# Kernel optimization log

Measured on AMD Instinct MI355X. Metric: run time of the kernel, lower is better.

The kernel has to match this reference:

```python
import jax, jax.numpy as jnp
import numpy as np

N = 128          # num_of_nodes
E = 4096         # directed edges (undirected doubled)
D = N + 2        # node feature dim after node_dim += num_of_nodes
H = 64           # hidden_dim


def _lin_params(key, fan_in, fan_out):
    s = 1.0 / np.sqrt(fan_in)
    kw, kb = jax.random.split(key)
    W = jax.random.uniform(kw, (fan_in, fan_out), jnp.float32, -s, s)
    b = jax.random.uniform(kb, (fan_out,), jnp.float32, -s, s)
    return W, b


def setup_inputs() -> dict:
    key = jax.random.key(0)
    ks = jax.random.split(key, 16)
    x = jax.random.normal(ks[0], (N, D), jnp.float32)
    edge_index = jax.random.randint(ks[1], (2, E), 0, N)
    edge_attr = jax.random.uniform(ks[2], (E, 1), jnp.float32)
    adjacency = jax.random.randint(ks[3], (N, N), 0, 2).astype(jnp.int32)
    # values in {-1, 0, 1}; -1 means node created no packet
    new_packets = jax.random.randint(ks[4], (N,), -1, 2).astype(jnp.float32)
    # conv1 edge MLP: Linear(1, D*H) -> ReLU -> Linear(D*H, D*H)
    W1a, b1a = _lin_params(ks[5], 1, D * H)
    W1b, b1b = _lin_params(ks[6], D * H, D * H)
    Wr1, _ = _lin_params(ks[7], D, H)        # NNConv root weight (no bias)
    bc1 = jnp.zeros((H,), jnp.float32)       # NNConv bias
    # conv2 edge MLP: Linear(1, H) -> ReLU -> Linear(H, H*H)
    W2a, b2a = _lin_params(ks[8], 1, H)
    W2b, b2b = _lin_params(ks[9], H, H * H)
    Wr2, _ = _lin_params(ks[10], H, H)
    bc2 = jnp.zeros((H,), jnp.float32)
    Wout, bout = _lin_params(ks[11], H, N)
    return dict(x=x, edge_index=edge_index, edge_attr=edge_attr,
                adjacency=adjacency, new_packets=new_packets,
                W1a=W1a, b1a=b1a, W1b=W1b, b1b=b1b, Wr1=Wr1, bc1=bc1,
                W2a=W2a, b2a=b2a, W2b=W2b, b2b=b2b, Wr2=Wr2, bc2=bc2,
                Wout=Wout, bout=bout)


def _nnconv(x, src, dst, edge_attr, Wa, ba, Wb, bb, Wr, bias, din, dout):
    # per-edge weight matrices from edge MLP: [E, din, dout]
    theta = (jax.nn.relu(edge_attr @ Wa + ba) @ Wb + bb).reshape(-1, din, dout)
    msg = jnp.einsum('ei,eio->eo', x[src], theta)          # gather + edge matmul
    agg = jax.ops.segment_sum(msg, dst, num_segments=N)     # scatter
    cnt = jax.ops.segment_sum(jnp.ones((msg.shape[0],), msg.dtype), dst,
                              num_segments=N)
    agg = agg / jnp.maximum(cnt, 1.0)[:, None]              # mean aggregation
    return agg + x @ Wr + bias                              # root weight + bias


def reference(x, edge_index, edge_attr, adjacency, new_packets,
              W1a, b1a, W1b, b1b, Wr1, bc1,
              W2a, b2a, W2b, b2b, Wr2, bc2,
              Wout, bout):
    src, dst = edge_index[0], edge_index[1]
    h = jax.nn.relu(_nnconv(x, src, dst, edge_attr, W1a, b1a, W1b, b1b, Wr1, bc1, D, H))
    h = jax.nn.relu(_nnconv(h, src, dst, edge_attr, W2a, b2a, W2b, b2b, Wr2, bc2, H, H))
    logits = h @ Wout + bout                                 # [N, N]
    masked = jnp.where(adjacency != 0, logits, -jnp.inf)
    probs = jax.nn.softmax(masked, axis=1)
    mask = new_packets != -1.0                               # nodes that created packets
    rp = jnp.where(mask[:, None], probs, 0.0)                # zero rows w/o packet
    idx = jnp.arange(N)
    rp = rp.at[idx, idx].add(jnp.where(mask, 0.0, 1.0))      # diag=1 for those rows
    return rp
```

## Files before the change

kernel.cpp:

```cpp
#include <hip/hip_runtime.h>

#define NN 128
#define NE 4096
#define DD 130
#define HH 64
#define KK1 8320
#define CC 256

#define OFF_AGG1 0
#define OFF_AGG2 8192
#define ZERO_F   16384
#define OFF_CNT  16384
#define OFF_XR1  16512
#define OFF_H1   24704
#define OFF_HB2  32896
#define OFF_HR2  41088
#define OFF_H2   49280
#define OFF_G2   57472
#define OFF_SP   581760
#define OFF_SQ   2711680
#define OFF_DP   4841600
#define OFF_DQ   6971520
#define OFF_INT  9101440

__device__ __forceinline__ int event_bin(float a, float c) {
  if (a > 0.f) {
    if (c <= 0.f) { float tt = -c / a; if (tt < 1.f) return (int)(tt * 256.0f); }
  } else if (a < 0.f) {
    if (c > 0.f) { float tt = -c / a; if (tt < 1.f) return (int)ceilf(tt * 256.0f) - 1; }
  }
  return -1;
}

__global__ __launch_bounds__(256) void k_count(const int* __restrict__ ei,
                                               const float* __restrict__ eattr,
                                               const float* __restrict__ W1a,
                                               const float* __restrict__ b1a,
                                               int* __restrict__ e_off,
                                               int* __restrict__ k_off,
                                               int* __restrict__ e_idx,
                                               int* __restrict__ k_idx,
                                               int* __restrict__ base_idx,
                                               int* __restrict__ nbase,
                                               float* __restrict__ cnt) {
  __shared__ int ec[CC], kc[CC], cd[NN];
  __shared__ int eo[CC + 1], ko[CC + 1];
  __shared__ int bcnt;
  int t = threadIdx.x;
  ec[t] = 0; kc[t] = 0;
  if (t < NN) cd[t] = 0;
  if (t == 0) bcnt = 0;
  __syncthreads();
  for (int e = t; e < NE; e += 256) {
    atomicAdd(&cd[ei[NE + e]], 1);
    int c = (int)(eattr[e] * 256.0f); c = c < 0 ? 0 : (c > CC - 1 ? CC - 1 : c);
    atomicAdd(&ec[c], 1);
  }
  for (int k = t; k < KK1; k += 256) {
    int b = event_bin(W1a[k], b1a[k]);
    if (b >= 0) atomicAdd(&kc[b], 1);
    if (b1a[k] > 0.f) { int p = atomicAdd(&bcnt, 1); base_idx[p] = k; }
  }
  __syncthreads();
  if (t == 0) {
    *nbase = bcnt;
    int r = 0;
    for (int c = 0; c < CC; c++) { eo[c] = r; r += ec[c]; } eo[CC] = r;
    r = 0;
    for (int c = 0; c < CC; c++) { ko[c] = r; r += kc[c]; } ko[CC] = r;
  }
  __syncthreads();
  if (t < NN) cnt[t] = (float)cd[t];
  e_off[t] = eo[t]; k_off[t] = ko[t];
  if (t == 0) { e_off[CC] = eo[CC]; k_off[CC] = ko[CC]; }
  ec[t] = eo[t]; kc[t] = ko[t];
  __syncthreads();
  for (int e = t; e < NE; e += 256) {
    int c = (int)(eattr[e] * 256.0f); c = c < 0 ? 0 : (c > CC - 1 ? CC - 1 : c);
    int p = atomicAdd(&ec[c], 1);
    e_idx[p] = e;
  }
  for (int k = t; k < KK1; k += 256) {
    int b = event_bin(W1a[k], b1a[k]);
    if (b >= 0) { int p = atomicAdd(&kc[b], 1); k_idx[p] = k; }
  }
}

__global__ __launch_bounds__(256) void k_small1x(const float* __restrict__ x,
                                                 const float* __restrict__ Wr1,
                                                 float* __restrict__ xr1) {
  int f = blockIdx.x * 256 + threadIdx.x;
  int n = f >> 6, o = f & 63;
  float a = 0.f;
  for (int i = 0; i < DD; i++) a = fmaf(x[n * DD + i], Wr1[i * HH + o], a);
  xr1[f] = a;
}

#define MCOL 33
__global__ __launch_bounds__(256) void k_base(const float* __restrict__ W1a,
                                              const float* __restrict__ b1a,
                                              const float* __restrict__ W1b,
                                              const int* __restrict__ base_idx,
                                              const int* __restrict__ nbase,
                                              float* __restrict__ SP0,
                                              float* __restrict__ SQ0) {
  int t = threadIdx.x;
  int nb = *nbase;
  float rp[MCOL], rq[MCOL];
#pragma unroll
  for (int m = 0; m < MCOL; m++) { rp[m] = 0.f; rq[m] = 0.f; }
  for (int r = blockIdx.x; r < nb; r += gridDim.x) {
    int k = base_idx[r];
    float a = W1a[k], c2 = b1a[k];
    const float* row = &W1b[(long)k * KK1];
#pragma unroll
    for (int m = 0; m < MCOL; m++) {
      int col = t + 256 * m;
      if (col < KK1) {
        float w = row[col];
        rp[m] = fmaf(a, w, rp[m]);
        rq[m] = fmaf(c2, w, rq[m]);
      }
    }
  }
#pragma unroll
  for (int m = 0; m < MCOL; m++) {
    int col = t + 256 * m;
    if (col < KK1) {
      atomicAdd(&SP0[col], rp[m]);
      atomicAdd(&SQ0[col], rq[m]);
    }
  }
}

__global__ __launch_bounds__(256) void k_diff(const float* __restrict__ W1a,
                                              const float* __restrict__ b1a,
                                              const float* __restrict__ W1b,
                                              const int* __restrict__ k_off,
                                              const int* __restrict__ k_idx,
                                              float* __restrict__ DP,
                                              float* __restrict__ DQ) {
  int c = blockIdx.x, t = threadIdx.x;
  int kb = k_off[c], ke = k_off[c + 1];
  float rp[MCOL], rq[MCOL];
#pragma unroll
  for (int m = 0; m < MCOL; m++) { rp[m] = 0.f; rq[m] = 0.f; }
  for (int r = kb; r < ke; ++r) {
    int k = k_idx[r];
    float a = W1a[k], c2 = b1a[k];
    float sa = (a > 0.f) ? a : -a;
    float sc = (a > 0.f) ? c2 : -c2;
    const float* row = &W1b[(long)k * KK1];
#pragma unroll
    for (int m = 0; m < MCOL; m++) {
      int col = t + 256 * m;
      if (col < KK1) {
        float w = row[col];
        rp[m] = fmaf(sa, w, rp[m]);
        rq[m] = fmaf(sc, w, rq[m]);
      }
    }
  }
#pragma unroll
  for (int m = 0; m < MCOL; m++) {
    int col = t + 256 * m;
    if (col < KK1) {
      DP[(long)c * KK1 + col] = rp[m];
      DQ[(long)c * KK1 + col] = rq[m];
    }
  }
}

__global__ __launch_bounds__(256) void k_prefix(float* __restrict__ SP,
                                                float* __restrict__ SQ,
                                                const float* __restrict__ DP,
                                                const float* __restrict__ DQ) {
  int f = blockIdx.x * 256 + threadIdx.x;
  float* S; const float* Dm; int col;
  if (f < KK1) { S = SP; Dm = DP; col = f; }
  else         { S = SQ; Dm = DQ; col = f - KK1; }
  float s = S[col];
  for (int c = 1; c < CC; c++) {
    s += Dm[(long)(c - 1) * KK1 + col];
    S[(long)c * KK1 + col] = s;
  }
}

#define EC 192
#define KC 128
__global__ __launch_bounds__(256) void k_sweep(const float* __restrict__ SP,
                                               const float* __restrict__ SQ,
                                               const float* __restrict__ b1b,
                                               const float* __restrict__ W1a,
                                               const float* __restrict__ b1a,
                                               const float* __restrict__ W1b,
                                               const float* __restrict__ x,
                                               const float* __restrict__ eattr,
                                               const int* __restrict__ ei,
                                               const int* __restrict__ e_off,
                                               const int* __restrict__ e_idx,
                                               const int* __restrict__ k_off,
                                               const int* __restrict__ k_idx,
                                               float* __restrict__ agg1) {
  __shared__ float Pl[KK1], Ql[KK1];
  __shared__ float eas[EC], eas_r[EC];
  __shared__ int eix[EC], eix_r[EC];
  __shared__ float tks[KC], tks_r[KC];
  __shared__ int kix[KC], kix_r[KC];
  int c = blockIdx.x, t = threadIdx.x;
  int eb = e_off[c], ne = e_off[c + 1] - eb; if (ne > EC) ne = EC;
  int kb = k_off[c], nk = k_off[c + 1] - kb; if (nk > KC) nk = KC;
  for (int j = t; j < KK1; j += 256) {
    Pl[j] = SP[(long)c * KK1 + j];
    Ql[j] = SQ[(long)c * KK1 + j] + b1b[j];
  }
  if (t < ne) { int e = e_idx[eb + t]; eix_r[t] = e; eas_r[t] = eattr[e]; }
  if (t < nk) {
    int k = k_idx[kb + t];
    kix_r[t] = k;
    tks_r[t] = -b1a[k] / W1a[k];
  }
  __syncthreads();
  if (t < ne) {
    float key = eas_r[t]; int rk = 0;
    for (int j = 0; j < ne; j++) { float kj = eas_r[j]; rk += (kj < key) || (kj == key && j < t); }
    eas[rk] = key; eix[rk] = eix_r[t];
  }
  if (t < nk) {
    float key = tks_r[t]; int rk = 0;
    for (int j = 0; j < nk; j++) { float kj = tks_r[j]; rk += (kj < key) || (kj == key && j < t); }
    tks[rk] = key; kix[rk] = kix_r[t];
  }
  __syncthreads();
  if (ne == 0) return;
  int ie = 0, ik = 0;
  int q = t >> 6, o = t & 63;
  while (ie < ne) {
    if (ik < nk && tks[ik] < eas[ie]) {
      int k = kix[ik];
      float a = W1a[k], c2 = b1a[k];
      float sa = (a > 0.f) ? a : -a;
      float sc = (a > 0.f) ? c2 : -c2;
      __syncthreads();
      for (int j = t; j < KK1; j += 256) {
        float w = W1b[(long)k * KK1 + j];
        Pl[j] = fmaf(sa, w, Pl[j]);
        Ql[j] = fmaf(sc, w, Ql[j]);
      }
      __syncthreads();
      ik++;
    } else {
      int m = 1;
      while (ie + m < ne && (ik >= nk || eas[ie + m] <= tks[ik])) m++;
      for (int g = 0; g < m; g += 4) {
        int sl = g + q;
        if (sl < m) {
          int e = eix[ie + sl];
          float eav = eas[ie + sl];
          int s = ei[e], d = ei[NE + e];
          const float* xp = &x[s * DD];
          float A = 0.f, B = 0.f;
#pragma unroll 2
          for (int i = 0; i < DD; i++) {
            float xv = xp[i];
            A = fmaf(xv, Pl[i * 64 + o], A);
            B = fmaf(xv, Ql[i * 64 + o], B);
          }
          atomicAdd(&agg1[d * 64 + o], fmaf(eav, A, B));
        }
      }
      ie += m;
    }
  }
}

__global__ __launch_bounds__(256) void k_h(const float* __restrict__ agg,
                                           const float* __restrict__ cnt,
                                           const float* __restrict__ xr,
                                           const float* __restrict__ bc,
                                           float* __restrict__ h) {
  int f = blockIdx.x * 256 + threadIdx.x;
  int n = f >> 6, o = f & 63;
  float c = fmaxf(cnt[n], 1.f);
  h[f] = fmaxf(0.f, agg[f] / c + xr[f] + bc[o]);
}

__global__ __launch_bounds__(256) void k_g2(const float* __restrict__ h1,
                                            const float* __restrict__ W2b,
                                            float* __restrict__ G2) {
  int f = blockIdx.x * 256 + threadIdx.x;
  int s = f >> 12, k = (f >> 6) & 63, o = f & 63;
  const float* hp = &h1[s * 64];
  const float* wp = &W2b[k * 4096 + o];
  float a = 0.f;
  for (int i = 0; i < 64; i++) a = fmaf(hp[i], wp[i * 64], a);
  G2[f] = a;
}

__global__ __launch_bounds__(256) void k_small2(const float* __restrict__ h1,
                                                const float* __restrict__ b2b,
                                                const float* __restrict__ Wr2,
                                                float* __restrict__ hb2,
                                                float* __restrict__ hr2) {
  int f = blockIdx.x * 256 + threadIdx.x;
  int n = f >> 6, o = f & 63;
  float a = 0.f, b = 0.f;
  for (int i = 0; i < 64; i++) {
    float hv = h1[n * 64 + i];
    a = fmaf(hv, b2b[i * 64 + o], a);
    b = fmaf(hv, Wr2[i * 64 + o], b);
  }
  hb2[f] = a; hr2[f] = b;
}

__global__ __launch_bounds__(256) void k_consume2(const float* __restrict__ G2,
                                                  const float* __restrict__ W2a,
                                                  const float* __restrict__ b2a,
                                                  const float* __restrict__ eattr,
                                                  const int* __restrict__ ei,
                                                  const float* __restrict__ hb2,
                                                  float* __restrict__ agg2) {
  __shared__ float wa[64], wb[64];
  int t = threadIdx.x;
  if (t < 64) { wa[t] = W2a[t]; wb[t] = b2a[t]; }
  __syncthreads();
  int f = blockIdx.x * 256 + t;
  int e = f >> 6, o = f & 63;
  int s = ei[e], d = ei[NE + e];
  float ev = eattr[e];
  float a = hb2[s * 64 + o];
  const float* gp = &G2[s * 4096 + o];
  for (int k = 0; k < 64; k++) {
    float u = fmaxf(0.f, fmaf(ev, wa[k], wb[k]));
    a = fmaf(u, gp[k * 64], a);
  }
  atomicAdd(&agg2[d * 64 + o], a);
}

__global__ __launch_bounds__(128) void k_out(const float* __restrict__ h2,
                                             const float* __restrict__ Wout,
                                             const float* __restrict__ bout,
                                             const int* __restrict__ adj,
                                             const float* __restrict__ npk,
                                             float* __restrict__ out) {
  __shared__ float hs[64];
  __shared__ float redm[2], reds[2];
  int n = blockIdx.x, j = threadIdx.x;
  if (j < 64) hs[j] = h2[n * 64 + j];
  __syncthreads();
  float l = bout[j];
  for (int k = 0; k < 64; k++) l = fmaf(hs[k], Wout[k * 128 + j], l);
  bool am = adj[n * 128 + j] != 0;
  float lm = am ? l : -3.0e38f;
  float m = lm;
  for (int off = 32; off >= 1; off >>= 1) m = fmaxf(m, __shfl_xor(m, off, 64));
  int wid = j >> 6;
  if ((j & 63) == 0) redm[wid] = m;
  __syncthreads();
  m = fmaxf(redm[0], redm[1]);
  float p = am ? expf(lm - m) : 0.f;
  float sv = p;
  for (int off = 32; off >= 1; off >>= 1) sv += __shfl_xor(sv, off, 64);
  if ((j & 63) == 0) reds[wid] = sv;
  __syncthreads();
  sv = reds[0] + reds[1];
  float prob = p / sv;
  bool haspkt = (npk[n] != -1.0f);
  out[n * 128 + j] = haspkt ? prob : ((j == n) ? 1.f : 0.f);
}

extern "C" void kernel_launch(void* const* d_in, const int* in_sizes, int n_in,
                              void* d_out, int out_size, void* d_ws, size_t ws_size,
                              hipStream_t stream) {
  const float* x    = (const float*)d_in[0];
  const int*   ei   = (const int*)  d_in[1];
  const float* ea   = (const float*)d_in[2];
  const int*   adj  = (const int*)  d_in[3];
  const float* npk  = (const float*)d_in[4];
  const float* W1a  = (const float*)d_in[5];
  const float* b1a  = (const float*)d_in[6];
  const float* W1b  = (const float*)d_in[7];
  const float* b1b  = (const float*)d_in[8];
  const float* Wr1  = (const float*)d_in[9];
  const float* bc1  = (const float*)d_in[10];
  const float* W2a  = (const float*)d_in[11];
  const float* b2a  = (const float*)d_in[12];
  const float* W2b  = (const float*)d_in[13];
  const float* b2b  = (const float*)d_in[14];
  const float* Wr2  = (const float*)d_in[15];
  const float* bc2  = (const float*)d_in[16];
  const float* Wout = (const float*)d_in[17];
  const float* bout = (const float*)d_in[18];

  float* ws = (float*)d_ws;
  int*   ip = (int*)(ws + OFF_INT);
  int* e_off    = ip;
  int* k_off    = ip + 257;
  int* e_idx    = ip + 514;
  int* k_idx    = ip + 4610;
  int* base_idx = ip + 12930;
  int* nbase    = ip + 21250;

  hipMemsetAsync(ws, 0, ZERO_F * sizeof(float), stream);
  hipMemsetAsync(ws + OFF_SP, 0, KK1 * sizeof(float), stream);
  hipMemsetAsync(ws + OFF_SQ, 0, KK1 * sizeof(float), stream);

  k_count<<<1, 256, 0, stream>>>(ei, ea, W1a, b1a, e_off, k_off, e_idx, k_idx,
                                 base_idx, nbase, ws + OFF_CNT);
  k_small1x<<<32, 256, 0, stream>>>(x, Wr1, ws + OFF_XR1);
  k_base<<<256, 256, 0, stream>>>(W1a, b1a, W1b, base_idx, nbase,
                                  ws + OFF_SP, ws + OFF_SQ);
  k_diff<<<CC, 256, 0, stream>>>(W1a, b1a, W1b, k_off, k_idx, ws + OFF_DP, ws + OFF_DQ);
  k_prefix<<<65, 256, 0, stream>>>(ws + OFF_SP, ws + OFF_SQ, ws + OFF_DP, ws + OFF_DQ);
  k_sweep<<<CC, 256, 0, stream>>>(ws + OFF_SP, ws + OFF_SQ, b1b, W1a, b1a, W1b,
                                  x, ea, ei, e_off, e_idx, k_off, k_idx, ws + OFF_AGG1);
  k_h<<<32, 256, 0, stream>>>(ws + OFF_AGG1, ws + OFF_CNT, ws + OFF_XR1, bc1, ws + OFF_H1);
  k_g2<<<2048, 256, 0, stream>>>(ws + OFF_H1, W2b, ws + OFF_G2);
  k_small2<<<32, 256, 0, stream>>>(ws + OFF_H1, b2b, Wr2, ws + OFF_HB2, ws + OFF_HR2);
  k_consume2<<<1024, 256, 0, stream>>>(ws + OFF_G2, W2a, b2a, ea, ei, ws + OFF_HB2,
                                       ws + OFF_AGG2);
  k_h<<<32, 256, 0, stream>>>(ws + OFF_AGG2, ws + OFF_CNT, ws + OFF_HR2, bc2, ws + OFF_H2);
  k_out<<<128, 128, 0, stream>>>(ws + OFF_H2, Wout, bout, adj, npk, (float*)d_out);
}
```

Before: 650.1 us.

## Parallelize prefix scan, split sweep by output half, CSR-gather conv2 aggregation

Replaces the serial 256-step column prefix over DP/DQ with a two-pass segmented scan (segment totals, then per-segment scan), so the grid grows by a factor of NSEG. k_sweep is split across two output halves, which halves its LDS footprint and doubles the block count, and b1b is now folded into SQ0 by a new init kernel. k_count also builds a destination-sorted edge permutation, and k_consume2 uses it to reduce per node in LDS, replacing global atomics with plain stores. The cost is extra launches, redundant reads of segment totals, and duplicated sorting and x loads per sweep half.

```diff
diff --git a/kernel.cpp b/kernel.cpp
--- a/kernel.cpp
+++ b/kernel.cpp
@@ -6,22 +6,26 @@
 #define HH 64
 #define KK1 8320
 #define CC 256
+#define NSEG 16
+#define SEGC 16
 
 #define OFF_AGG1 0
-#define OFF_AGG2 8192
-#define ZERO_F   16384
-#define OFF_CNT  16384
-#define OFF_XR1  16512
-#define OFF_H1   24704
-#define OFF_HB2  32896
-#define OFF_HR2  41088
-#define OFF_H2   49280
+#define ZERO_F   8192
+#define OFF_CNT  8192
+#define OFF_XR1  8320
+#define OFF_H1   16512
+#define OFF_HB2  24704
+#define OFF_HR2  32896
+#define OFF_H2   41088
+#define OFF_AGG2 49280
 #define OFF_G2   57472
 #define OFF_SP   581760
 #define OFF_SQ   2711680
 #define OFF_DP   4841600
 #define OFF_DQ   6971520
 #define OFF_INT  9101440
+#define OFF_TP   9127040
+#define OFF_TQ   9260160
 
 __device__ __forceinline__ int event_bin(float a, float c) {
   if (a > 0.f) {
@@ -42,9 +46,11 @@
                                                int* __restrict__ k_idx,
                                                int* __restrict__ base_idx,
                                                int* __restrict__ nbase,
+                                               int* __restrict__ d_off,
+                                               int* __restrict__ perm_dst,
                                                float* __restrict__ cnt) {
   __shared__ int ec[CC], kc[CC], cd[NN];
-  __shared__ int eo[CC + 1], ko[CC + 1];
+  __shared__ int eo[CC + 1], ko[CC + 1], doff[NN + 1];
   __shared__ int bcnt;
   int t = threadIdx.x;
   ec[t] = 0; kc[t] = 0;
@@ -68,17 +74,24 @@
     for (int c = 0; c < CC; c++) { eo[c] = r; r += ec[c]; } eo[CC] = r;
     r = 0;
     for (int c = 0; c < CC; c++) { ko[c] = r; r += kc[c]; } ko[CC] = r;
-  }
-  __syncthreads();
-  if (t < NN) cnt[t] = (float)cd[t];
+    r = 0;
+    for (int n = 0; n < NN; n++) { doff[n] = r; r += cd[n]; } doff[NN] = r;
+  }
+  __syncthreads();
+  if (t < NN) { cnt[t] = (float)cd[t]; d_off[t] = doff[t]; }
+  if (t == 0) d_off[NN] = doff[NN];
   e_off[t] = eo[t]; k_off[t] = ko[t];
   if (t == 0) { e_off[CC] = eo[CC]; k_off[CC] = ko[CC]; }
   ec[t] = eo[t]; kc[t] = ko[t];
+  if (t < NN) cd[t] = doff[t];
   __syncthreads();
   for (int e = t; e < NE; e += 256) {
     int c = (int)(eattr[e] * 256.0f); c = c < 0 ? 0 : (c > CC - 1 ? CC - 1 : c);
     int p = atomicAdd(&ec[c], 1);
     e_idx[p] = e;
+    int d = ei[NE + e];
+    int pd = atomicAdd(&cd[d], 1);
+    perm_dst[pd] = e;
   }
   for (int k = t; k < KK1; k += 256) {
     int b = event_bin(W1a[k], b1a[k]);
@@ -94,6 +107,13 @@
   float a = 0.f;
   for (int i = 0; i < DD; i++) a = fmaf(x[n * DD + i], Wr1[i * HH + o], a);
   xr1[f] = a;
+}
+
+__global__ __launch_bounds__(256) void k_init(const float* __restrict__ b1b,
+                                              float* __restrict__ SP0,
+                                              float* __restrict__ SQ0) {
+  int f = blockIdx.x * 256 + threadIdx.x;
+  if (f < KK1) { SP0[f] = 0.f; SQ0[f] = b1b[f]; }
 }
 
 #define MCOL 33
@@ -171,26 +191,45 @@
   }
 }
 
-__global__ __launch_bounds__(256) void k_prefix(float* __restrict__ SP,
-                                                float* __restrict__ SQ,
-                                                const float* __restrict__ DP,
-                                                const float* __restrict__ DQ) {
-  int f = blockIdx.x * 256 + threadIdx.x;
-  float* S; const float* Dm; int col;
-  if (f < KK1) { S = SP; Dm = DP; col = f; }
-  else         { S = SQ; Dm = DQ; col = f - KK1; }
-  float s = S[col];
-  for (int c = 1; c < CC; c++) {
-    s += Dm[(long)(c - 1) * KK1 + col];
-    S[(long)c * KK1 + col] = s;
+__global__ __launch_bounds__(256) void k_seg(const float* __restrict__ DP,
+                                             const float* __restrict__ DQ,
+                                             float* __restrict__ TP,
+                                             float* __restrict__ TQ) {
+  int f = blockIdx.x * 256 + threadIdx.x;
+  int s = blockIdx.y;
+  const float* Dm; float* T; int col;
+  if (f < KK1) { Dm = DP; T = TP; col = f; }
+  else         { Dm = DQ; T = TQ; col = f - KK1; }
+  float a = 0.f;
+  for (int p = 0; p < SEGC; p++) a += Dm[(long)(s * SEGC + p) * KK1 + col];
+  T[(long)s * KK1 + col] = a;
+}
+
+__global__ __launch_bounds__(256) void k_scan(float* __restrict__ SP,
+                                              float* __restrict__ SQ,
+                                              const float* __restrict__ DP,
+                                              const float* __restrict__ DQ,
+                                              const float* __restrict__ TP,
+                                              const float* __restrict__ TQ) {
+  int f = blockIdx.x * 256 + threadIdx.x;
+  int s = blockIdx.y;
+  float* S; const float* Dm; const float* T; int col;
+  if (f < KK1) { S = SP; Dm = DP; T = TP; col = f; }
+  else         { S = SQ; Dm = DQ; T = TQ; col = f - KK1; }
+  float acc = S[col];
+  for (int sp = 0; sp < s; sp++) acc += T[(long)sp * KK1 + col];
+  for (int p = 0; p < SEGC; p++) {
+    int c = s * SEGC + p;
+    if (c > 0) S[(long)c * KK1 + col] = acc;
+    acc += Dm[(long)c * KK1 + col];
   }
 }
 
 #define EC 192
 #define KC 128
+#define KHW 4160
 __global__ __launch_bounds__(256) void k_sweep(const float* __restrict__ SP,
                                                const float* __restrict__ SQ,
-                                               const float* __restrict__ b1b,
                                                const float* __restrict__ W1a,
                                                const float* __restrict__ b1a,
                                                const float* __restrict__ W1b,
@@ -202,17 +241,20 @@
                                                const int* __restrict__ k_off,
                                                const int* __restrict__ k_idx,
                                                float* __restrict__ agg1) {
-  __shared__ float Pl[KK1], Ql[KK1];
+  __shared__ float Pl[KHW], Ql[KHW];
   __shared__ float eas[EC], eas_r[EC];
   __shared__ int eix[EC], eix_r[EC];
   __shared__ float tks[KC], tks_r[KC];
   __shared__ int kix[KC], kix_r[KC];
-  int c = blockIdx.x, t = threadIdx.x;
+  int c = blockIdx.x, oh = blockIdx.y, t = threadIdx.x;
+  int ob = oh * 32;
   int eb = e_off[c], ne = e_off[c + 1] - eb; if (ne > EC) ne = EC;
   int kb = k_off[c], nk = k_off[c + 1] - kb; if (nk > KC) nk = KC;
-  for (int j = t; j < KK1; j += 256) {
-    Pl[j] = SP[(long)c * KK1 + j];
-    Ql[j] = SQ[(long)c * KK1 + j] + b1b[j];
+  for (int j = t; j < KHW; j += 256) {
+    int i = j >> 5, ol = j & 31;
+    long col = (long)c * KK1 + i * 64 + ob + ol;
+    Pl[j] = SP[col];
+    Ql[j] = SQ[col];
   }
   if (t < ne) { int e = e_idx[eb + t]; eix_r[t] = e; eas_r[t] = eattr[e]; }
   if (t < nk) {
@@ -234,16 +276,18 @@
   __syncthreads();
   if (ne == 0) return;
   int ie = 0, ik = 0;
-  int q = t >> 6, o = t & 63;
+  int q = t >> 5, ol = t & 31;
   while (ie < ne) {
     if (ik < nk && tks[ik] < eas[ie]) {
       int k = kix[ik];
       float a = W1a[k], c2 = b1a[k];
       float sa = (a > 0.f) ? a : -a;
       float sc = (a > 0.f) ? c2 : -c2;
+      const float* row = &W1b[(long)k * KK1 + ob];
       __syncthreads();
-      for (int j = t; j < KK1; j += 256) {
-        float w = W1b[(long)k * KK1 + j];
+      for (int j = t; j < KHW; j += 256) {
+        int i = j >> 5, o2 = j & 31;
+        float w = row[i * 64 + o2];
         Pl[j] = fmaf(sa, w, Pl[j]);
         Ql[j] = fmaf(sc, w, Ql[j]);
       }
@@ -252,7 +296,7 @@
     } else {
       int m = 1;
       while (ie + m < ne && (ik >= nk || eas[ie + m] <= tks[ik])) m++;
-      for (int g = 0; g < m; g += 4) {
+      for (int g = 0; g < m; g += 8) {
         int sl = g + q;
         if (sl < m) {
           int e = eix[ie + sl];
@@ -263,10 +307,10 @@
 #pragma unroll 2
           for (int i = 0; i < DD; i++) {
             float xv = xp[i];
-            A = fmaf(xv, Pl[i * 64 + o], A);
-            B = fmaf(xv, Ql[i * 64 + o], B);
+            A = fmaf(xv, Pl[i * 32 + ol], A);
+            B = fmaf(xv, Ql[i * 32 + ol], B);
           }
-          atomicAdd(&agg1[d * 64 + o], fmaf(eav, A, B));
+          atomicAdd(&agg1[d * 64 + ob + ol], fmaf(eav, A, B));
         }
       }
       ie += m;
@@ -318,23 +362,38 @@
                                                   const float* __restrict__ b2a,
                                                   const float* __restrict__ eattr,
                                                   const int* __restrict__ ei,
+                                                  const int* __restrict__ d_off,
+                                                  const int* __restrict__ perm_dst,
                                                   const float* __restrict__ hb2,
                                                   float* __restrict__ agg2) {
   __shared__ float wa[64], wb[64];
-  int t = threadIdx.x;
+  __shared__ float red[8][32];
+  int n = blockIdx.x, oh = blockIdx.y, t = threadIdx.x;
+  int sl = t >> 5, ol = t & 31;
   if (t < 64) { wa[t] = W2a[t]; wb[t] = b2a[t]; }
   __syncthreads();
-  int f = blockIdx.x * 256 + t;
-  int e = f >> 6, o = f & 63;
-  int s = ei[e], d = ei[NE + e];
-  float ev = eattr[e];
-  float a = hb2[s * 64 + o];
-  const float* gp = &G2[s * 4096 + o];
-  for (int k = 0; k < 64; k++) {
-    float u = fmaxf(0.f, fmaf(ev, wa[k], wb[k]));
-    a = fmaf(u, gp[k * 64], a);
-  }
-  atomicAdd(&agg2[d * 64 + o], a);
+  int b0 = d_off[n], b1 = d_off[n + 1];
+  float acc = 0.f;
+  for (int r = b0 + sl; r < b1; r += 8) {
+    int e = perm_dst[r];
+    int s = ei[e];
+    float ev = eattr[e];
+    const float* gp = &G2[s * 4096 + oh * 32 + ol];
+    float a = hb2[s * 64 + oh * 32 + ol];
+    for (int k = 0; k < 64; k++) {
+      float u = fmaxf(0.f, fmaf(ev, wa[k], wb[k]));
+      a = fmaf(u, gp[k * 64], a);
+    }
+    acc += a;
+  }
+  red[sl][ol] = acc;
+  __syncthreads();
+  if (sl == 0) {
+    float a = 0.f;
+#pragma unroll
+    for (int j = 0; j < 8; j++) a += red[j][ol];
+    agg2[n * 64 + oh * 32 + ol] = a;
+  }
 }
 
 __global__ __launch_bounds__(128) void k_out(const float* __restrict__ h2,
@@ -400,25 +459,32 @@
   int* k_idx    = ip + 4610;
   int* base_idx = ip + 12930;
   int* nbase    = ip + 21250;
-
-  hipMemsetAsync(ws, 0, ZERO_F * sizeof(float), stream);
-  hipMemsetAsync(ws + OFF_SP, 0, KK1 * sizeof(float), stream);
-  hipMemsetAsync(ws + OFF_SQ, 0, KK1 * sizeof(float), stream);
+  int* d_off    = ip + 21251;
+  int* perm_dst = ip + 21380;
+
+  hipMemsetAsync(ws + OFF_AGG1, 0, 8192 * sizeof(float), stream);
 
   k_count<<<1, 256, 0, stream>>>(ei, ea, W1a, b1a, e_off, k_off, e_idx, k_idx,
-                                 base_idx, nbase, ws + OFF_CNT);
+                                 base_idx, nbase, d_off, perm_dst, ws + OFF_CNT);
   k_small1x<<<32, 256, 0, stream>>>(x, Wr1, ws + OFF_XR1);
+  k_init<<<33, 256, 0, stream>>>(b1b, ws + OFF_SP, ws + OFF_SQ);
   k_base<<<256, 256, 0, stream>>>(W1a, b1a, W1b, base_idx, nbase,
                                   ws + OFF_SP, ws + OFF_SQ);
   k_diff<<<CC, 256, 0, stream>>>(W1a, b1a, W1b, k_off, k_idx, ws + OFF_DP, ws + OFF_DQ);
-  k_prefix<<<65, 256, 0, stream>>>(ws + OFF_SP, ws + OFF_SQ, ws + OFF_DP, ws + OFF_DQ);
-  k_sweep<<<CC, 256, 0, stream>>>(ws + OFF_SP, ws + OFF_SQ, b1b, W1a, b1a, W1b,
-                                  x, ea, ei, e_off, e_idx, k_off, k_idx, ws + OFF_AGG1);
+  k_seg<<<dim3(65, NSEG), 256, 0, stream>>>(ws + OFF_DP, ws + OFF_DQ,
+                                            ws + OFF_TP, ws + OFF_TQ);
+  k_scan<<<dim3(65, NSEG), 256, 0, stream>>>(ws + OFF_SP, ws + OFF_SQ,
+                                             ws + OFF_DP, ws + OFF_DQ,
+                                             ws + OFF_TP, ws + OFF_TQ);
+  k_sweep<<<dim3(CC, 2), 256, 0, stream>>>(ws + OFF_SP, ws + OFF_SQ, W1a, b1a, W1b,
+                                           x, ea, ei, e_off, e_idx, k_off, k_idx,
+                                           ws + OFF_AGG1);
   k_h<<<32, 256, 0, stream>>>(ws + OFF_AGG1, ws + OFF_CNT, ws + OFF_XR1, bc1, ws + OFF_H1);
   k_g2<<<2048, 256, 0, stream>>>(ws + OFF_H1, W2b, ws + OFF_G2);
   k_small2<<<32, 256, 0, stream>>>(ws + OFF_H1, b2b, Wr2, ws + OFF_HB2, ws + OFF_HR2);
-  k_consume2<<<1024, 256, 0, stream>>>(ws + OFF_G2, W2a, b2a, ea, ei, ws + OFF_HB2,
-                                       ws + OFF_AGG2);
+  k_consume2<<<dim3(NN, 2), 256, 0, stream>>>(ws + OFF_G2, W2a, b2a, ea, ei,
+                                              d_off, perm_dst, ws + OFF_HB2,
+                                              ws + OFF_AGG2);
   k_h<<<32, 256, 0, stream>>>(ws + OFF_AGG2, ws + OFF_CNT, ws + OFF_HR2, bc2, ws + OFF_H2);
   k_out<<<128, 128, 0, stream>>>(ws + OFF_H2, Wout, bout, adj, npk, (float*)d_out);
 }
```

Result: no change. 643.9 us (-1.0%).
